# Optimization experiments

Hardware: AMD Instinct MI355X
Metric: run time of the kernel (lower is better)

## Reference

```python
import jax, jax.numpy as jnp
import numpy as np

N = 50000      # nodes
E = 800000     # edges
D = 128        # node_dim
H = 4          # heads
C = 64         # hidden_dim per head
B = 64         # graphs in batch
OUT = 10       # output_dim
SLOPE = 0.2    # GATConv leaky_relu negative slope (PyG default)


def gat_conv(x, src, dst, W, a_src, a_dst, bias, concat):
    """One PyG-style GATConv layer. src/dst already include self-loops."""
    n = x.shape[0]
    h = (x @ W).reshape(n, H, C)                       # [N,H,C]
    al_s = jnp.sum(h * a_src, axis=-1)                  # [N,H]
    al_d = jnp.sum(h * a_dst, axis=-1)                  # [N,H]
    e = jax.nn.leaky_relu(al_s[src] + al_d[dst], SLOPE)  # [E+N,H]
    m = jax.ops.segment_max(e, dst, num_segments=n)      # per-target-node max
    e = jnp.exp(e - m[dst])
    den = jax.ops.segment_sum(e, dst, num_segments=n)
    alpha = e / (den[dst] + 1e-16)                       # [E+N,H]
    msg = h[src] * alpha[:, :, None]                     # [E+N,H,C]
    out = jax.ops.segment_sum(msg, dst, num_segments=n)  # [N,H,C]
    out = out.reshape(n, H * C) if concat else out.mean(axis=1)
    return out + bias


def gat_forward(x, edge_index, batch, W0, b0, as0, ad0, W1, b1, as1, ad1,
                W2, b2, as2, ad2, pW1, pb1, pW2, pb2):
    n = x.shape[0]
    loop = jnp.arange(n, dtype=edge_index.dtype)
    src = jnp.concatenate([edge_index[0], loop])
    dst = jnp.concatenate([edge_index[1], loop])

    h = gat_conv(x, src, dst, W0, as0, ad0, b0, concat=True)
    h = jax.nn.elu(h)                                    # dropout = identity (eval)
    h = gat_conv(h, src, dst, W1, as1, ad1, b1, concat=True)
    h = jax.nn.elu(h)
    h = gat_conv(h, src, dst, W2, as2, ad2, b2, concat=False)  # [N,C]

    # global_mean_pool
    sums = jax.ops.segment_sum(h, batch, num_segments=B)        # [B,C]
    cnt = jax.ops.segment_sum(jnp.ones((n,), h.dtype), batch, num_segments=B)
    pooled = sums / jnp.maximum(cnt, 1.0)[:, None]

    # predictor MLP
    z = jax.nn.relu(pooled @ pW1 + pb1)
    return z @ pW2 + pb2                                        # [B,OUT]


def setup_inputs() -> dict:
    key = jax.random.key(0)
    ks = jax.random.split(key, 24)
    gl = lambda k, shp, fan: (jax.random.normal(k, shp, jnp.float32) / np.float32(np.sqrt(fan)))
    x = jax.random.normal(ks[0], (N, D), jnp.float32)
    edge_index = jax.random.randint(ks[1], (2, E), 0, N, dtype=jnp.int32)
    batch = jnp.sort(jax.random.randint(ks[2], (N,), 0, B, dtype=jnp.int32))
    return dict(
        x=x, edge_index=edge_index, batch=batch,
        W0=gl(ks[3], (D, H * C), D), b0=jnp.zeros((H * C,), jnp.float32),
        as0=gl(ks[4], (H, C), C), ad0=gl(ks[5], (H, C), C),
        W1=gl(ks[6], (H * C, H * C), H * C), b1=jnp.zeros((H * C,), jnp.float32),
        as1=gl(ks[7], (H, C), C), ad1=gl(ks[8], (H, C), C),
        W2=gl(ks[9], (H * C, H * C), H * C), b2=jnp.zeros((C,), jnp.float32),
        as2=gl(ks[10], (H, C), C), ad2=gl(ks[11], (H, C), C),
        pW1=gl(ks[12], (C, C // 2), C), pb1=jnp.zeros((C // 2,), jnp.float32),
        pW2=gl(ks[13], (C // 2, OUT), C // 2), pb2=jnp.zeros((OUT,), jnp.float32),
    )


def reference(x, edge_index, batch, W0, b0, as0, ad0, W1, b1, as1, ad1,
              W2, b2, as2, ad2, pW1, pb1, pW2, pb2):
    return gat_forward(x, edge_index, batch, W0, b0, as0, ad0, W1, b1, as1, ad1,
                       W2, b2, as2, ad2, pW1, pb1, pW2, pb2)
```

## Files before the change

### kernel.cpp

```cpp
#include <hip/hip_runtime.h>
#include <hip/hip_fp16.h>
#include <cstdint>

#define N_NODES 50000
#define E_EDGES 800000
#define HC 256
#define B_GR 64
#define OUT_DIM 10
#define SLOPE 0.2f
#define NBLK_SCAN ((N_NODES + 255) / 256)

using f16x8 = __attribute__((ext_vector_type(8))) _Float16;
using f32x4 = __attribute__((ext_vector_type(4))) float;

__global__ void wsplit_kernel(const float* __restrict__ W, _Float16* __restrict__ wt_hi,
                              _Float16* __restrict__ wt_lo, int K) {
    int i = blockIdx.x * 256 + threadIdx.x;
    if (i >= K * 256) return;
    int k = i >> 8, n = i & 255;
    float v = W[i];
    _Float16 h = (_Float16)v;
    _Float16 l = (_Float16)(v - (float)h);
    int oidx = ((((k >> 5) * 256 + n) * 4) + ((k >> 3) & 3)) * 8 + (k & 7);
    wt_hi[oidx] = h;
    wt_lo[oidx] = l;
}

template<int K>
__global__ __launch_bounds__(256) void gemm_mfma(const float* __restrict__ A,
        const _Float16* __restrict__ wt_hi, const _Float16* __restrict__ wt_lo,
        __half* __restrict__ h_half,
        const float* __restrict__ a_src, const float* __restrict__ a_dst,
        float* __restrict__ al_s, float* __restrict__ al_d, int M) {
    __shared__ _Float16 a_hi[64][64];
    __shared__ _Float16 a_lo[64][64];
    int tid = threadIdx.x;
    int w = tid >> 6;
    int l = tid & 63;
    int rr = l & 15;
    int kg = l >> 4;
    int row0 = blockIdx.x * 64;
    int lrow = tid >> 2;
    int lgp  = (tid & 3) * 2;

    f32x4 acc[4][4] = {};

    for (int k0 = 0; k0 < K; k0 += 64) {
        if (k0 > 0) __syncthreads();
        int gr = row0 + lrow;
#pragma unroll
        for (int gi = 0; gi < 2; ++gi) {
            int g = lgp + gi;
            float vv[8];
            if (gr < M) {
                float4 p = *(const float4*)&A[(size_t)gr * K + k0 + g * 8];
                float4 q = *(const float4*)&A[(size_t)gr * K + k0 + g * 8 + 4];
                vv[0] = p.x; vv[1] = p.y; vv[2] = p.z; vv[3] = p.w;
                vv[4] = q.x; vv[5] = q.y; vv[6] = q.z; vv[7] = q.w;
            } else {
#pragma unroll
                for (int j = 0; j < 8; ++j) vv[j] = 0.f;
            }
            f16x8 vh, vl;
#pragma unroll
            for (int j = 0; j < 8; ++j) {
                _Float16 hh = (_Float16)vv[j];
                vh[j] = hh;
                vl[j] = (_Float16)(vv[j] - (float)hh);
            }
            int gs = g ^ (lrow & 7);
            *(f16x8*)&a_hi[lrow][gs * 8] = vh;
            *(f16x8*)&a_lo[lrow][gs * 8] = vl;
        }
        __syncthreads();
#pragma unroll
        for (int c = 0; c < 2; ++c) {
            f16x8 ah[4], alo[4];
#pragma unroll
            for (int fm = 0; fm < 4; ++fm) {
                int row = fm * 16 + rr;
                int gsw = ((c * 4 + kg) ^ (row & 7));
                ah[fm]  = *(const f16x8*)&a_hi[row][gsw * 8];
                alo[fm] = *(const f16x8*)&a_lo[row][gsw * 8];
            }
            int chunk = (k0 >> 5) + c;
#pragma unroll
            for (int fn = 0; fn < 4; ++fn) {
                int col = w * 64 + fn * 16 + rr;
                size_t boff = (((size_t)chunk * 256 + col) * 4 + kg) * 8;
                f16x8 bh = *(const f16x8*)&wt_hi[boff];
                f16x8 bl = *(const f16x8*)&wt_lo[boff];
#pragma unroll
                for (int fm = 0; fm < 4; ++fm) {
                    acc[fm][fn] = __builtin_amdgcn_mfma_f32_16x16x32_f16(ah[fm],  bh, acc[fm][fn], 0, 0, 0);
                    acc[fm][fn] = __builtin_amdgcn_mfma_f32_16x16x32_f16(ah[fm],  bl, acc[fm][fn], 0, 0, 0);
                    acc[fm][fn] = __builtin_amdgcn_mfma_f32_16x16x32_f16(alo[fm], bh, acc[fm][fn], 0, 0, 0);
                }
            }
        }
    }

    int head = w;
    float asv[4], adv[4];
#pragma unroll
    for (int fn = 0; fn < 4; ++fn) {
        asv[fn] = a_src[head * 64 + fn * 16 + rr];
        adv[fn] = a_dst[head * 64 + fn * 16 + rr];
    }
#pragma unroll
    for (int fm = 0; fm < 4; ++fm) {
#pragma unroll
        for (int r = 0; r < 4; ++r) {
            int row = fm * 16 + kg * 4 + r;
            int gr = row0 + row;
            float ps = acc[fm][0][r] * asv[0] + acc[fm][1][r] * asv[1]
                     + acc[fm][2][r] * asv[2] + acc[fm][3][r] * asv[3];
            float pd = acc[fm][0][r] * adv[0] + acc[fm][1][r] * adv[1]
                     + acc[fm][2][r] * adv[2] + acc[fm][3][r] * adv[3];
#pragma unroll
            for (int off = 1; off < 16; off <<= 1) {
                ps += __shfl_xor(ps, off, 64);
                pd += __shfl_xor(pd, off, 64);
            }
            if (gr < M) {
#pragma unroll
                for (int fn = 0; fn < 4; ++fn)
                    h_half[(size_t)gr * HC + w * 64 + fn * 16 + rr] = __float2half(acc[fm][fn][r]);
                if (rr == 0) {
                    al_s[gr * 4 + head] = ps;
                    al_d[gr * 4 + head] = pd;
                }
            }
        }
    }
}

__global__ void init_cnt(int* cnt) {
    int i = blockIdx.x * blockDim.x + threadIdx.x;
    if (i < N_NODES) cnt[i] = 1;
}
__global__ void hist_kernel(const int* __restrict__ dsts, int* cnt) {
    int i = blockIdx.x * blockDim.x + threadIdx.x;
    if (i < E_EDGES) atomicAdd(&cnt[dsts[i]], 1);
}
__global__ __launch_bounds__(256) void scan_bsum(const int* __restrict__ cnt,
                                                 int* __restrict__ bsum) {
    __shared__ int ws[4];
    int t = threadIdx.x;
    int i = blockIdx.x * 256 + t;
    int v = (i < N_NODES) ? cnt[i] : 0;
#pragma unroll
    for (int off = 1; off < 64; off <<= 1) v += __shfl_xor(v, off, 64);
    if ((t & 63) == 0) ws[t >> 6] = v;
    __syncthreads();
    if (t == 0) bsum[blockIdx.x] = ws[0] + ws[1] + ws[2] + ws[3];
}
__global__ __launch_bounds__(256) void scan_boff(const int* __restrict__ bsum,
                                                 int* __restrict__ boff) {
    __shared__ int s[256];
    int t = threadIdx.x;
    int v = (t < NBLK_SCAN) ? bsum[t] : 0;
    s[t] = v;
    __syncthreads();
    for (int off = 1; off < 256; off <<= 1) {
        int u = (t >= off) ? s[t - off] : 0;
        __syncthreads();
        s[t] += u;
        __syncthreads();
    }
    if (t < NBLK_SCAN) boff[t] = s[t] - v;
}
__global__ __launch_bounds__(256) void scan_final(const int* __restrict__ cnt,
        const int* __restrict__ boff, int* __restrict__ row_ptr,
        int* __restrict__ cursor) {
    __shared__ int s[256];
    int b = blockIdx.x, t = threadIdx.x;
    int i = b * 256 + t;
    int v = (i < N_NODES) ? cnt[i] : 0;
    s[t] = v;
    __syncthreads();
    for (int off = 1; off < 256; off <<= 1) {
        int u = (t >= off) ? s[t - off] : 0;
        __syncthreads();
        s[t] += u;
        __syncthreads();
    }
    int rp = boff[b] + s[t] - v;
    if (i < N_NODES) { row_ptr[i] = rp; cursor[i] = rp; }
    if (i == N_NODES - 1) row_ptr[N_NODES] = rp + v;
}
__global__ void scatter_kernel(const int* __restrict__ srcs, const int* __restrict__ dsts,
                               int* cursor, int* col) {
    int i = blockIdx.x * blockDim.x + threadIdx.x;
    if (i >= E_EDGES + N_NODES) return;
    int s, d;
    if (i < E_EDGES) { s = srcs[i]; d = dsts[i]; }
    else             { s = d = i - E_EDGES; }
    int pos = atomicAdd(&cursor[d], 1);
    col[pos] = s;
}

__global__ __launch_bounds__(256) void agg_kernel(const __half* __restrict__ hh,
        const float* __restrict__ al_s, const float* __restrict__ al_d,
        const int* __restrict__ row_ptr, const int* __restrict__ col,
        const float* __restrict__ bias, float* __restrict__ out, int mode) {
    __shared__ int   lds_col[4][64];
    __shared__ float lds_alpha[4][64][4];
    int wid  = threadIdx.x >> 6;
    int lane = threadIdx.x & 63;
    int hf   = lane >> 5;
    int ln   = lane & 31;
    int nodeA = blockIdx.x * 8 + wid * 2;
    int nodeB = nodeA + 1;
    int sA = row_ptr[nodeA], eA = row_ptr[nodeA + 1];
    int sB = row_ptr[nodeB], eB = row_ptr[nodeB + 1];
    int degA = eA - sA, degB = eB - sB;

    if (degA <= 32 && degB <= 32) {
        int node  = hf ? nodeB : nodeA;
        int start = hf ? sB : sA;
        int deg   = hf ? degB : degA;
        int degmax = max(degA, degB);
        const float4 ald = *(const float4*)&al_d[node * 4];
        bool active = ln < deg;
        int s = active ? col[start + ln] : 0;
        float4 as = *(const float4*)&al_s[s * 4];
        float e0 = as.x + ald.x; e0 = e0 > 0.f ? e0 : SLOPE * e0;
        float e1 = as.y + ald.y; e1 = e1 > 0.f ? e1 : SLOPE * e1;
        float e2 = as.z + ald.z; e2 = e2 > 0.f ? e2 : SLOPE * e2;
        float e3 = as.w + ald.w; e3 = e3 > 0.f ? e3 : SLOPE * e3;
        float m0 = active ? e0 : -1e30f, m1 = active ? e1 : -1e30f;
        float m2 = active ? e2 : -1e30f, m3 = active ? e3 : -1e30f;
#pragma unroll
        for (int off = 1; off < 32; off <<= 1) {
            m0 = fmaxf(m0, __shfl_xor(m0, off, 64));
            m1 = fmaxf(m1, __shfl_xor(m1, off, 64));
            m2 = fmaxf(m2, __shfl_xor(m2, off, 64));
            m3 = fmaxf(m3, __shfl_xor(m3, off, 64));
        }
        float x0 = active ? expf(e0 - m0) : 0.f;
        float x1 = active ? expf(e1 - m1) : 0.f;
        float x2 = active ? expf(e2 - m2) : 0.f;
        float x3 = active ? expf(e3 - m3) : 0.f;
        float d0 = x0, d1 = x1, d2 = x2, d3 = x3;
#pragma unroll
        for (int off = 1; off < 32; off <<= 1) {
            d0 += __shfl_xor(d0, off, 64);
            d1 += __shfl_xor(d1, off, 64);
            d2 += __shfl_xor(d2, off, 64);
            d3 += __shfl_xor(d3, off, 64);
        }
        float4 a4;
        a4.x = x0 / (d0 + 1e-16f); a4.y = x1 / (d1 + 1e-16f);
        a4.z = x2 / (d2 + 1e-16f); a4.w = x3 / (d3 + 1e-16f);
        int e = hf * 32 + ln;
        lds_col[wid][e] = s;
        *(float4*)&lds_alpha[wid][e][0] = a4;
        int head = ln >> 3;
        int ch0 = ln * 8;
        float acc[8] = {0.f, 0.f, 0.f, 0.f, 0.f, 0.f, 0.f, 0.f};
        int ebase = hf * 32;
        for (int t0 = 0; t0 < degmax; t0 += 4) {
            float wv[4]; float4 raw[4];
#pragma unroll
            for (int k = 0; k < 4; ++k) {
                int t = t0 + k;
                int tt = min(t, deg - 1);
                int s2 = lds_col[wid][ebase + tt];
                wv[k] = (t < deg) ? lds_alpha[wid][ebase + tt][head] : 0.f;
                raw[k] = *(const float4*)&hh[(size_t)s2 * HC + ch0];
            }
#pragma unroll
            for (int k = 0; k < 4; ++k) {
                const __half2* hp = (const __half2*)&raw[k];
                float2 f0 = __half22float2(hp[0]);
                float2 f1 = __half22float2(hp[1]);
                float2 f2 = __half22float2(hp[2]);
                float2 f3 = __half22float2(hp[3]);
                acc[0] = fmaf(wv[k], f0.x, acc[0]); acc[1] = fmaf(wv[k], f0.y, acc[1]);
                acc[2] = fmaf(wv[k], f1.x, acc[2]); acc[3] = fmaf(wv[k], f1.y, acc[3]);
                acc[4] = fmaf(wv[k], f2.x, acc[4]); acc[5] = fmaf(wv[k], f2.y, acc[5]);
                acc[6] = fmaf(wv[k], f3.x, acc[6]); acc[7] = fmaf(wv[k], f3.y, acc[7]);
            }
        }
        if (mode == 0) {
            float b8[8];
            *(float4*)&b8[0] = *(const float4*)&bias[ch0];
            *(float4*)&b8[4] = *(const float4*)&bias[ch0 + 4];
            float v[8];
#pragma unroll
            for (int j = 0; j < 8; ++j) {
                float t = acc[j] + b8[j];
                v[j] = t > 0.f ? t : expm1f(t);
            }
            *(float4*)&out[(size_t)node * HC + ch0]     = *(float4*)&v[0];
            *(float4*)&out[(size_t)node * HC + ch0 + 4] = *(float4*)&v[4];
        } else {
#pragma unroll
            for (int j = 0; j < 8; ++j) {
                acc[j] += __shfl_xor(acc[j], 8, 64);
                acc[j] += __shfl_xor(acc[j], 16, 64);
            }
            if (ln < 8) {
                float v[8];
#pragma unroll
                for (int j = 0; j < 8; ++j)
                    v[j] = acc[j] * 0.25f + bias[ln * 8 + j];
                *(float4*)&out[(size_t)node * 64 + ln * 8]     = *(float4*)&v[0];
                *(float4*)&out[(size_t)node * 64 + ln * 8 + 4] = *(float4*)&v[4];
            }
        }
        return;
    }

    for (int nn = 0; nn < 2; ++nn) {
        int node = nodeA + nn;
        int start = row_ptr[node], end = row_ptr[node + 1];
        int deg = end - start;
        const float4 ald = *(const float4*)&al_d[node * 4];
        int head = lane >> 4;
        float ald_h = head == 0 ? ald.x : head == 1 ? ald.y : head == 2 ? ald.z : ald.w;
        float ax = 0.f, ay = 0.f, az = 0.f, aw = 0.f;

        if (deg <= 64) {
            int j = start + lane;
            bool active = j < end;
            int s = active ? col[j] : 0;
            float4 as = *(const float4*)&al_s[s * 4];
            float e0 = as.x + ald.x; e0 = e0 > 0.f ? e0 : SLOPE * e0;
            float e1 = as.y + ald.y; e1 = e1 > 0.f ? e1 : SLOPE * e1;
            float e2 = as.z + ald.z; e2 = e2 > 0.f ? e2 : SLOPE * e2;
            float e3 = as.w + ald.w; e3 = e3 > 0.f ? e3 : SLOPE * e3;
            float m0 = active ? e0 : -1e30f, m1 = active ? e1 : -1e30f;
            float m2 = active ? e2 : -1e30f, m3 = active ? e3 : -1e30f;
#pragma unroll
            for (int off = 1; off < 64; off <<= 1) {
                m0 = fmaxf(m0, __shfl_xor(m0, off, 64));
                m1 = fmaxf(m1, __shfl_xor(m1, off, 64));
                m2 = fmaxf(m2, __shfl_xor(m2, off, 64));
                m3 = fmaxf(m3, __shfl_xor(m3, off, 64));
            }
            float x0 = active ? expf(e0 - m0) : 0.f;
            float x1 = active ? expf(e1 - m1) : 0.f;
            float x2 = active ? expf(e2 - m2) : 0.f;
            float x3 = active ? expf(e3 - m3) : 0.f;
            float d0 = x0, d1 = x1, d2 = x2, d3 = x3;
#pragma unroll
            for (int off = 1; off < 64; off <<= 1) {
                d0 += __shfl_xor(d0, off, 64);
                d1 += __shfl_xor(d1, off, 64);
                d2 += __shfl_xor(d2, off, 64);
                d3 += __shfl_xor(d3, off, 64);
            }
            float4 a4;
            a4.x = x0 / (d0 + 1e-16f); a4.y = x1 / (d1 + 1e-16f);
            a4.z = x2 / (d2 + 1e-16f); a4.w = x3 / (d3 + 1e-16f);
            lds_col[wid][lane] = s;
            *(float4*)&lds_alpha[wid][lane][0] = a4;
            for (int t0 = 0; t0 < deg; t0 += 8) {
                int nr = deg - t0;
                float wv[8]; float2 raw[8];
#pragma unroll
                for (int k = 0; k < 8; ++k) {
                    if (k < nr) {
                        int s2 = lds_col[wid][t0 + k];
                        wv[k] = lds_alpha[wid][t0 + k][head];
                        raw[k] = *(const float2*)&hh[(size_t)s2 * HC + lane * 4];
                    } else {
                        wv[k] = 0.f;
                        raw[k] = make_float2(0.f, 0.f);
                    }
                }
#pragma unroll
                for (int k = 0; k < 8; ++k) {
                    float2 f0 = __half22float2(*(__half2*)&raw[k].x);
                    float2 f1 = __half22float2(*(__half2*)&raw[k].y);
                    ax = fmaf(wv[k], f0.x, ax); ay = fmaf(wv[k], f0.y, ay);
                    az = fmaf(wv[k], f1.x, az); aw = fmaf(wv[k], f1.y, aw);
                }
            }
        } else {
            float m0 = -1e30f, m1 = -1e30f, m2 = -1e30f, m3 = -1e30f;
            for (int j = start + lane; j < end; j += 64) {
                int s = col[j];
                float4 as = *(const float4*)&al_s[s * 4];
                float e0 = as.x + ald.x; e0 = e0 > 0.f ? e0 : SLOPE * e0;
                float e1 = as.y + ald.y; e1 = e1 > 0.f ? e1 : SLOPE * e1;
                float e2 = as.z + ald.z; e2 = e2 > 0.f ? e2 : SLOPE * e2;
                float e3 = as.w + ald.w; e3 = e3 > 0.f ? e3 : SLOPE * e3;
                m0 = fmaxf(m0, e0); m1 = fmaxf(m1, e1);
                m2 = fmaxf(m2, e2); m3 = fmaxf(m3, e3);
            }
#pragma unroll
            for (int off = 1; off < 64; off <<= 1) {
                m0 = fmaxf(m0, __shfl_xor(m0, off, 64));
                m1 = fmaxf(m1, __shfl_xor(m1, off, 64));
                m2 = fmaxf(m2, __shfl_xor(m2, off, 64));
                m3 = fmaxf(m3, __shfl_xor(m3, off, 64));
            }
            float d0 = 0.f, d1 = 0.f, d2 = 0.f, d3 = 0.f;
            for (int j = start + lane; j < end; j += 64) {
                int s = col[j];
                float4 as = *(const float4*)&al_s[s * 4];
                float e0 = as.x + ald.x; e0 = e0 > 0.f ? e0 : SLOPE * e0;
                float e1 = as.y + ald.y; e1 = e1 > 0.f ? e1 : SLOPE * e1;
                float e2 = as.z + ald.z; e2 = e2 > 0.f ? e2 : SLOPE * e2;
                float e3 = as.w + ald.w; e3 = e3 > 0.f ? e3 : SLOPE * e3;
                d0 += expf(e0 - m0); d1 += expf(e1 - m1);
                d2 += expf(e2 - m2); d3 += expf(e3 - m3);
            }
#pragma unroll
            for (int off = 1; off < 64; off <<= 1) {
                d0 += __shfl_xor(d0, off, 64);
                d1 += __shfl_xor(d1, off, 64);
                d2 += __shfl_xor(d2, off, 64);
                d3 += __shfl_xor(d3, off, 64);
            }
            float inv0 = 1.f / (d0 + 1e-16f), inv1 = 1.f / (d1 + 1e-16f);
            float inv2 = 1.f / (d2 + 1e-16f), inv3 = 1.f / (d3 + 1e-16f);
            float m_h   = head == 0 ? m0   : head == 1 ? m1   : head == 2 ? m2   : m3;
            float inv_h = head == 0 ? inv0 : head == 1 ? inv1 : head == 2 ? inv2 : inv3;
            for (int jb = start; jb < end; jb += 64) {
                int j = jb + lane;
                int cs = (j < end) ? col[j] : 0;
                int cnt2 = min(64, end - jb);
                for (int t = 0; t < cnt2; ++t) {
                    int s = __shfl(cs, t, 64);
                    float als2 = al_s[s * 4 + head];
                    float e = als2 + ald_h; e = e > 0.f ? e : SLOPE * e;
                    float wv = expf(e - m_h) * inv_h;
                    float2 raw = *(const float2*)&hh[(size_t)s * HC + lane * 4];
                    float2 f0 = __half22float2(*(__half2*)&raw.x);
                    float2 f1 = __half22float2(*(__half2*)&raw.y);
                    ax = fmaf(wv, f0.x, ax); ay = fmaf(wv, f0.y, ay);
                    az = fmaf(wv, f1.x, az); aw = fmaf(wv, f1.y, aw);
                }
            }
        }

        if (mode == 0) {
            float4 b4 = *(const float4*)&bias[lane * 4];
            float vx = ax + b4.x; vx = vx > 0.f ? vx : expm1f(vx);
            float vy = ay + b4.y; vy = vy > 0.f ? vy : expm1f(vy);
            float vz = az + b4.z; vz = vz > 0.f ? vz : expm1f(vz);
            float vw = aw + b4.w; vw = vw > 0.f ? vw : expm1f(vw);
            float4 v = make_float4(vx, vy, vz, vw);
            *(float4*)&out[(size_t)node * HC + lane * 4] = v;
        } else {
#pragma unroll
            for (int off = 16; off < 64; off <<= 1) {
                ax += __shfl_xor(ax, off, 64);
                ay += __shfl_xor(ay, off, 64);
                az += __shfl_xor(az, off, 64);
                aw += __shfl_xor(aw, off, 64);
            }
            if (lane < 16) {
                float4 b4 = *(const float4*)&bias[lane * 4];
                float4 v = make_float4(ax * 0.25f + b4.x, ay * 0.25f + b4.y,
                                       az * 0.25f + b4.z, aw * 0.25f + b4.w);
                *(float4*)&out[(size_t)node * 64 + lane * 4] = v;
            }
        }
    }
}

__global__ void pool_zero(float* __restrict__ pooled) {
    int i = blockIdx.x * blockDim.x + threadIdx.x;
    if (i < B_GR * 64) pooled[i] = 0.f;
}

__global__ __launch_bounds__(256) void pool_kernel(const float* __restrict__ act,
        const int* __restrict__ batch, float* __restrict__ pooled) {
    int b = blockIdx.x;
    int chunk = blockIdx.y;
    int warp = threadIdx.x >> 6;
    int lane = threadIdx.x & 63;
    int lo = 0, hi = N_NODES;
    while (lo < hi) { int mid = (lo + hi) >> 1; if (batch[mid] < b) lo = mid + 1; else hi = mid; }
    int s = lo;
    lo = 0; hi = N_NODES;
    while (lo < hi) { int mid = (lo + hi) >> 1; if (batch[mid] < b + 1) lo = mid + 1; else hi = mid; }
    int e = lo;
    float sum = 0.f;
    for (int n = s + chunk * 4 + warp; n < e; n += 64)
        sum += act[(size_t)n * 64 + lane];
    atomicAdd(&pooled[b * 64 + lane], sum);
}

__global__ __launch_bounds__(64) void mlp_kernel(const float* __restrict__ pooled,
        const int* __restrict__ batch,
        const float* __restrict__ pW1, const float* __restrict__ pb1,
        const float* __restrict__ pW2, const float* __restrict__ pb2,
        float* __restrict__ outp) {
    __shared__ float p[64];
    __shared__ float z[32];
    int b = blockIdx.x, t = threadIdx.x;
    int lo = 0, hi = N_NODES;
    while (lo < hi) { int mid = (lo + hi) >> 1; if (batch[mid] < b) lo = mid + 1; else hi = mid; }
    int s = lo;
    lo = 0; hi = N_NODES;
    while (lo < hi) { int mid = (lo + hi) >> 1; if (batch[mid] < b + 1) lo = mid + 1; else hi = mid; }
    int e = lo;
    float inv = 1.f / (float)max(e - s, 1);
    p[t] = pooled[b * 64 + t] * inv;
    __syncthreads();
    if (t < 32) {
        float s2 = pb1[t];
        for (int c = 0; c < 64; ++c) s2 += p[c] * pW1[c * 32 + t];
        z[t] = s2 > 0.f ? s2 : 0.f;
    }
    __syncthreads();
    if (t < OUT_DIM) {
        float s2 = pb2[t];
        for (int k = 0; k < 32; ++k) s2 += z[k] * pW2[k * 10 + t];
        outp[b * 10 + t] = s2;
    }
}

extern "C" void kernel_launch(void* const* d_in, const int* in_sizes, int n_in,
                              void* d_out, int out_size, void* d_ws, size_t ws_size,
                              hipStream_t stream) {
    const float* x    = (const float*)d_in[0];
    const int*   ei   = (const int*)d_in[1];
    const int*   batch= (const int*)d_in[2];
    const float* W0   = (const float*)d_in[3];
    const float* b0   = (const float*)d_in[4];
    const float* as0  = (const float*)d_in[5];
    const float* ad0  = (const float*)d_in[6];
    const float* W1   = (const float*)d_in[7];
    const float* b1   = (const float*)d_in[8];
    const float* as1  = (const float*)d_in[9];
    const float* ad1  = (const float*)d_in[10];
    const float* W2   = (const float*)d_in[11];
    const float* b2   = (const float*)d_in[12];
    const float* as2  = (const float*)d_in[13];
    const float* ad2  = (const float*)d_in[14];
    const float* pW1  = (const float*)d_in[15];
    const float* pb1  = (const float*)d_in[16];
    const float* pW2  = (const float*)d_in[17];
    const float* pb2  = (const float*)d_in[18];
    float* out = (float*)d_out;

    char* ws = (char*)d_ws;
    size_t off = 0;
    auto alloc = [&](size_t bytes) -> void* {
        void* p = ws + off;
        off += (bytes + 255) & ~(size_t)255;
        return p;
    };
    __half* h_half = (__half*)alloc((size_t)N_NODES * HC * 2);
    float* act    = (float*)alloc((size_t)N_NODES * HC * 4);
    float* als    = (float*)alloc((size_t)N_NODES * 4 * 4);
    float* ald    = (float*)alloc((size_t)N_NODES * 4 * 4);
    int*   cnt    = (int*)alloc((size_t)N_NODES * 4);
    int*   row_ptr= (int*)alloc((size_t)(N_NODES + 1) * 4);
    int*   cursor = (int*)alloc((size_t)N_NODES * 4);
    int*   col    = (int*)alloc((size_t)(E_EDGES + N_NODES) * 4);
    float* pooled = (float*)alloc((size_t)B_GR * 64 * 4);
    int*   bsum   = (int*)alloc((size_t)NBLK_SCAN * 4);
    int*   boff   = (int*)alloc((size_t)NBLK_SCAN * 4);
    _Float16* w0h = (_Float16*)alloc((size_t)128 * 256 * 2);
    _Float16* w0l = (_Float16*)alloc((size_t)128 * 256 * 2);
    _Float16* w1h = (_Float16*)alloc((size_t)256 * 256 * 2);
    _Float16* w1l = (_Float16*)alloc((size_t)256 * 256 * 2);
    _Float16* w2h = (_Float16*)alloc((size_t)256 * 256 * 2);
    _Float16* w2l = (_Float16*)alloc((size_t)256 * 256 * 2);

    const int* srcs = ei;
    const int* dsts = ei + E_EDGES;

    wsplit_kernel<<<(128 * 256 + 255) / 256, 256, 0, stream>>>(W0, w0h, w0l, 128);
    wsplit_kernel<<<(256 * 256 + 255) / 256, 256, 0, stream>>>(W1, w1h, w1l, 256);
    wsplit_kernel<<<(256 * 256 + 255) / 256, 256, 0, stream>>>(W2, w2h, w2l, 256);

    init_cnt<<<(N_NODES + 255) / 256, 256, 0, stream>>>(cnt);
    hist_kernel<<<(E_EDGES + 255) / 256, 256, 0, stream>>>(dsts, cnt);
    scan_bsum<<<NBLK_SCAN, 256, 0, stream>>>(cnt, bsum);
    scan_boff<<<1, 256, 0, stream>>>(bsum, boff);
    scan_final<<<NBLK_SCAN, 256, 0, stream>>>(cnt, boff, row_ptr, cursor);
    scatter_kernel<<<(E_EDGES + N_NODES + 255) / 256, 256, 0, stream>>>(srcs, dsts, cursor, col);

    int gblk = (N_NODES + 63) / 64;
    int nblk = (N_NODES + 7) / 8;

    gemm_mfma<128><<<gblk, 256, 0, stream>>>(x, w0h, w0l, h_half, as0, ad0, als, ald, N_NODES);
    agg_kernel<<<nblk, 256, 0, stream>>>(h_half, als, ald, row_ptr, col, b0, act, 0);
    gemm_mfma<256><<<gblk, 256, 0, stream>>>(act, w1h, w1l, h_half, as1, ad1, als, ald, N_NODES);
    agg_kernel<<<nblk, 256, 0, stream>>>(h_half, als, ald, row_ptr, col, b1, act, 0);
    gemm_mfma<256><<<gblk, 256, 0, stream>>>(act, w2h, w2l, h_half, as2, ad2, als, ald, N_NODES);
    agg_kernel<<<nblk, 256, 0, stream>>>(h_half, als, ald, row_ptr, col, b2, act, 1);

    pool_zero<<<(B_GR * 64 + 255) / 256, 256, 0, stream>>>(pooled);
    dim3 pgrid(B_GR, 16);
    pool_kernel<<<pgrid, 256, 0, stream>>>(act, batch, pooled);
    mlp_kernel<<<B_GR, 64, 0, stream>>>(pooled, batch, pW1, pb1, pW2, pb2, out);
}
```

Measured before the change: 445.0 us.

## Store inter-layer activations in fp16 and add fp16-input GEMM with direct-to-LDS loads

The aggregation kernel now writes ELU-activated hidden features as fp16 rather than fp32, which halves the activation write traffic and the read traffic of the next layer's GEMM. A new gemm_fp16 kernel loads the fp16 A tile straight into a swizzled LDS buffer with global_load_lds and skips the in-kernel hi/lo split of A, so it issues two MFMAs per step instead of the split scheme's larger count. The final layer still writes fp32 for pooling. The cost is that activations are rounded to fp16 and lose precision, which may affect agreement with the fp32 reference.

```diff
diff --git a/kernel.cpp b/kernel.cpp
--- a/kernel.cpp
+++ b/kernel.cpp
@@ -12,6 +12,10 @@
 
 using f16x8 = __attribute__((ext_vector_type(8))) _Float16;
 using f32x4 = __attribute__((ext_vector_type(4))) float;
+
+#define GLOAD_LDS16(gsrc, ldst) \
+    __builtin_amdgcn_global_load_lds((const __attribute__((address_space(1))) void*)(gsrc), \
+        (__attribute__((address_space(3))) void*)(ldst), 16, 0, 0)
 
 __global__ void wsplit_kernel(const float* __restrict__ W, _Float16* __restrict__ wt_hi,
                               _Float16* __restrict__ wt_lo, int K) {
@@ -135,6 +139,96 @@
     }
 }
 
+template<int K>
+__global__ __launch_bounds__(256) void gemm_fp16(const _Float16* __restrict__ A,
+        const _Float16* __restrict__ wt_hi, const _Float16* __restrict__ wt_lo,
+        __half* __restrict__ h_half,
+        const float* __restrict__ a_src, const float* __restrict__ a_dst,
+        float* __restrict__ al_s, float* __restrict__ al_d, int M) {
+    __shared__ _Float16 a16[64][64];
+    int tid = threadIdx.x;
+    int w = tid >> 6;
+    int l = tid & 63;
+    int rr = l & 15;
+    int kg = l >> 4;
+    int row0 = blockIdx.x * 64;
+    int srow = tid >> 3;
+    int sgs  = tid & 7;
+
+    f32x4 acc[4][4] = {};
+
+    for (int k0 = 0; k0 < K; k0 += 64) {
+        if (k0 > 0) __syncthreads();
+#pragma unroll
+        for (int i = 0; i < 2; ++i) {
+            int row = i * 32 + srow;
+            int g   = sgs ^ (row & 7);
+            int gr  = min(row0 + row, M - 1);
+            const _Float16* src = &A[(size_t)gr * K + k0 + g * 8];
+            char* ldsbase = (char*)&a16[0][0] + i * 4096 + w * 1024;
+            GLOAD_LDS16(src, ldsbase);
+        }
+        __syncthreads();
+#pragma unroll
+        for (int c = 0; c < 2; ++c) {
+            f16x8 ah[4];
+#pragma unroll
+            for (int fm = 0; fm < 4; ++fm) {
+                int row = fm * 16 + rr;
+                int gsw = ((c * 4 + kg) ^ (row & 7));
+                ah[fm] = *(const f16x8*)&a16[row][gsw * 8];
+            }
+            int chunk = (k0 >> 5) + c;
+#pragma unroll
+            for (int fn = 0; fn < 4; ++fn) {
+                int col = w * 64 + fn * 16 + rr;
+                size_t boff = (((size_t)chunk * 256 + col) * 4 + kg) * 8;
+                f16x8 bh = *(const f16x8*)&wt_hi[boff];
+                f16x8 bl = *(const f16x8*)&wt_lo[boff];
+#pragma unroll
+                for (int fm = 0; fm < 4; ++fm) {
+                    acc[fm][fn] = __builtin_amdgcn_mfma_f32_16x16x32_f16(ah[fm], bh, acc[fm][fn], 0, 0, 0);
+                    acc[fm][fn] = __builtin_amdgcn_mfma_f32_16x16x32_f16(ah[fm], bl, acc[fm][fn], 0, 0, 0);
+                }
+            }
+        }
+    }
+
+    int head = w;
+    float asv[4], adv[4];
+#pragma unroll
+    for (int fn = 0; fn < 4; ++fn) {
+        asv[fn] = a_src[head * 64 + fn * 16 + rr];
+        adv[fn] = a_dst[head * 64 + fn * 16 + rr];
+    }
+#pragma unroll
+    for (int fm = 0; fm < 4; ++fm) {
+#pragma unroll
+        for (int r = 0; r < 4; ++r) {
+            int row = fm * 16 + kg * 4 + r;
+            int gr = row0 + row;
+            float ps = acc[fm][0][r] * asv[0] + acc[fm][1][r] * asv[1]
+                     + acc[fm][2][r] * asv[2] + acc[fm][3][r] * asv[3];
+            float pd = acc[fm][0][r] * adv[0] + acc[fm][1][r] * adv[1]
+                     + acc[fm][2][r] * adv[2] + acc[fm][3][r] * adv[3];
+#pragma unroll
+            for (int off = 1; off < 16; off <<= 1) {
+                ps += __shfl_xor(ps, off, 64);
+                pd += __shfl_xor(pd, off, 64);
+            }
+            if (gr < M) {
+#pragma unroll
+                for (int fn = 0; fn < 4; ++fn)
+                    h_half[(size_t)gr * HC + w * 64 + fn * 16 + rr] = __float2half(acc[fm][fn][r]);
+                if (rr == 0) {
+                    al_s[gr * 4 + head] = ps;
+                    al_d[gr * 4 + head] = pd;
+                }
+            }
+        }
+    }
+}
+
 __global__ void init_cnt(int* cnt) {
     int i = blockIdx.x * blockDim.x + threadIdx.x;
     if (i < N_NODES) cnt[i] = 1;
@@ -203,7 +297,8 @@
 __global__ __launch_bounds__(256) void agg_kernel(const __half* __restrict__ hh,
         const float* __restrict__ al_s, const float* __restrict__ al_d,
         const int* __restrict__ row_ptr, const int* __restrict__ col,
-        const float* __restrict__ bias, float* __restrict__ out, int mode) {
+        const float* __restrict__ bias, _Float16* __restrict__ out_h,
+        float* __restrict__ out_f, int mode) {
     __shared__ int   lds_col[4][64];
     __shared__ float lds_alpha[4][64][4];
     int wid  = threadIdx.x >> 6;
@@ -287,14 +382,13 @@
             float b8[8];
             *(float4*)&b8[0] = *(const float4*)&bias[ch0];
             *(float4*)&b8[4] = *(const float4*)&bias[ch0 + 4];
-            float v[8];
+            _Float16 v[8];
 #pragma unroll
             for (int j = 0; j < 8; ++j) {
                 float t = acc[j] + b8[j];
-                v[j] = t > 0.f ? t : expm1f(t);
-            }
-            *(float4*)&out[(size_t)node * HC + ch0]     = *(float4*)&v[0];
-            *(float4*)&out[(size_t)node * HC + ch0 + 4] = *(float4*)&v[4];
+                v[j] = (_Float16)(t > 0.f ? t : expm1f(t));
+            }
+            *(float4*)&out_h[(size_t)node * HC + ch0] = *(float4*)v;
         } else {
 #pragma unroll
             for (int j = 0; j < 8; ++j) {
@@ -306,8 +400,8 @@
 #pragma unroll
                 for (int j = 0; j < 8; ++j)
                     v[j] = acc[j] * 0.25f + bias[ln * 8 + j];
-                *(float4*)&out[(size_t)node * 64 + ln * 8]     = *(float4*)&v[0];
-                *(float4*)&out[(size_t)node * 64 + ln * 8 + 4] = *(float4*)&v[4];
+                *(float4*)&out_f[(size_t)node * 64 + ln * 8]     = *(float4*)&v[0];
+                *(float4*)&out_f[(size_t)node * 64 + ln * 8 + 4] = *(float4*)&v[4];
             }
         }
         return;
@@ -444,8 +538,8 @@
             float vy = ay + b4.y; vy = vy > 0.f ? vy : expm1f(vy);
             float vz = az + b4.z; vz = vz > 0.f ? vz : expm1f(vz);
             float vw = aw + b4.w; vw = vw > 0.f ? vw : expm1f(vw);
-            float4 v = make_float4(vx, vy, vz, vw);
-            *(float4*)&out[(size_t)node * HC + lane * 4] = v;
+            _Float16 v[4] = {(_Float16)vx, (_Float16)vy, (_Float16)vz, (_Float16)vw};
+            *(float2*)&out_h[(size_t)node * HC + lane * 4] = *(float2*)v;
         } else {
 #pragma unroll
             for (int off = 16; off < 64; off <<= 1) {
@@ -458,7 +552,7 @@
                 float4 b4 = *(const float4*)&bias[lane * 4];
                 float4 v = make_float4(ax * 0.25f + b4.x, ay * 0.25f + b4.y,
                                        az * 0.25f + b4.z, aw * 0.25f + b4.w);
-                *(float4*)&out[(size_t)node * 64 + lane * 4] = v;
+                *(float4*)&out_f[(size_t)node * 64 + lane * 4] = v;
             }
         }
     }
@@ -548,8 +642,9 @@
         off += (bytes + 255) & ~(size_t)255;
         return p;
     };
-    __half* h_half = (__half*)alloc((size_t)N_NODES * HC * 2);
-    float* act    = (float*)alloc((size_t)N_NODES * HC * 4);
+    __half*    h_half = (__half*)alloc((size_t)N_NODES * HC * 2);
+    _Float16*  act_h  = (_Float16*)alloc((size_t)N_NODES * HC * 2);
+    float*     act_f  = (float*)alloc((size_t)N_NODES * 64 * 4);
     float* als    = (float*)alloc((size_t)N_NODES * 4 * 4);
     float* ald    = (float*)alloc((size_t)N_NODES * 4 * 4);
     int*   cnt    = (int*)alloc((size_t)N_NODES * 4);
@@ -584,14 +679,14 @@
     int nblk = (N_NODES + 7) / 8;
 
     gemm_mfma<128><<<gblk, 256, 0, stream>>>(x, w0h, w0l, h_half, as0, ad0, als, ald, N_NODES);
-    agg_kernel<<<nblk, 256, 0, stream>>>(h_half, als, ald, row_ptr, col, b0, act, 0);
-    gemm_mfma<256><<<gblk, 256, 0, stream>>>(act, w1h, w1l, h_half, as1, ad1, als, ald, N_NODES);
-    agg_kernel<<<nblk, 256, 0, stream>>>(h_half, als, ald, row_ptr, col, b1, act, 0);
-    gemm_mfma<256><<<gblk, 256, 0, stream>>>(act, w2h, w2l, h_half, as2, ad2, als, ald, N_NODES);
-    agg_kernel<<<nblk, 256, 0, stream>>>(h_half, als, ald, row_ptr, col, b2, act, 1);
+    agg_kernel<<<nblk, 256, 0, stream>>>(h_half, als, ald, row_ptr, col, b0, act_h, act_f, 0);
+    gemm_fp16<256><<<gblk, 256, 0, stream>>>(act_h, w1h, w1l, h_half, as1, ad1, als, ald, N_NODES);
+    agg_kernel<<<nblk, 256, 0, stream>>>(h_half, als, ald, row_ptr, col, b1, act_h, act_f, 0);
+    gemm_fp16<256><<<gblk, 256, 0, stream>>>(act_h, w2h, w2l, h_half, as2, ad2, als, ald, N_NODES);
+    agg_kernel<<<nblk, 256, 0, stream>>>(h_half, als, ald, row_ptr, col, b2, act_h, act_f, 1);
 
     pool_zero<<<(B_GR * 64 + 255) / 256, 256, 0, stream>>>(pooled);
     dim3 pgrid(B_GR, 16);
-    pool_kernel<<<pgrid, 256, 0, stream>>>(act, batch, pooled);
+    pool_kernel<<<pgrid, 256, 0, stream>>>(act_f, batch, pooled);
     mlp_kernel<<<B_GR, 64, 0, stream>>>(pooled, batch, pW1, pb1, pW2, pb2, out);
 }
```

Result: faster. 425.3 us (-4.4%).
